# Kernel tuning notes

Measured on AMD Instinct MI355X. Metric: run time of the kernel, lower is better.

Reference implementation:

```python
import math
import jax, jax.numpy as jnp
import numpy as np

B, T, C, H = 2, 2048, 1024, 16
D = C // H


def _slopes(n):
    def p2(m):
        start = 2 ** (-(2 ** -(math.log2(m) - 3)))
        return [start * start ** i for i in range(m)]
    if math.log2(n).is_integer():
        return p2(n)
    c = 2 ** math.floor(math.log2(n))
    return p2(c) + _slopes(2 * c)[0::2][: n - c]


def setup_inputs() -> dict:
    key = jax.random.key(0)
    ks = jax.random.split(key, 9)
    std = 0.02
    x = jax.random.normal(ks[0], (B, T, C), dtype=jnp.float32)
    Wq = std * jax.random.normal(ks[1], (C, C), dtype=jnp.float32)
    Wk = std * jax.random.normal(ks[2], (C, C), dtype=jnp.float32)
    Wv = std * jax.random.normal(ks[3], (C, C), dtype=jnp.float32)
    # fc_resid init: std 0.02/sqrt(num_layers)
    Wo = (std / math.sqrt(24.0)) * jax.random.normal(ks[4], (C, C), dtype=jnp.float32)
    bq = jnp.zeros((C,), jnp.float32)
    bk = jnp.zeros((C,), jnp.float32)
    bv = jnp.zeros((C,), jnp.float32)
    bo = jnp.zeros((C,), jnp.float32)
    return {"x": x, "Wq": Wq, "bq": bq, "Wk": Wk, "bk": bk,
            "Wv": Wv, "bv": bv, "Wo": Wo, "bo": bo}


def reference(x, Wq, bq, Wk, bk, Wv, bv, Wo, bo):
    # projections -> [B, T, H, D]
    q = (x @ Wq + bq).reshape(B, T, H, D)
    k = (x @ Wk + bk).reshape(B, T, H, D)
    v = (x @ Wv + bv).reshape(B, T, H, D)

    scale = 1.0 / math.sqrt(D)
    att = jnp.einsum("bqhd,bkhd->bhqk", q, k) * scale  # [B,H,T,T]

    slopes = jnp.asarray(_slopes(H), dtype=jnp.float32)  # [H]
    i = jnp.arange(T)
    rel = i[None, :] - i[None, :].T  # rel[i,j] = j - i
    causal = rel <= 0  # j <= i
    # alibi bias: -tril(i - j) = tril(j - i), scaled per head
    alibi = slopes[:, None, None] * jnp.where(causal, rel, 0).astype(jnp.float32)

    att = att + alibi[None]  # broadcast over batch
    att = jnp.where(causal[None, None], att, -jnp.inf)
    att = jax.nn.softmax(att, axis=-1)

    y = jnp.einsum("bhqk,bkhd->bqhd", att, v).reshape(B, T, C)
    return y @ Wo + bo  # dropout p=0 (eval) is identity
```

## Files before the change

### kernel.cpp

```cpp
#include <hip/hip_runtime.h>
#include <hip/hip_bf16.h>

typedef __bf16 bf16;
typedef __bf16 bf16x4 __attribute__((ext_vector_type(4)));
typedef __bf16 bf16x8 __attribute__((ext_vector_type(8)));
typedef float floatx4 __attribute__((ext_vector_type(4)));
typedef short short4_ __attribute__((ext_vector_type(4)));

#define B_ 2
#define T_ 2048
#define C_ 1024
#define H_ 16
#define D_ 64
#define M_ 4096
#define QK_LD 2048

__device__ __forceinline__ void load_lds16(const void* g, void* l) {
  __builtin_amdgcn_global_load_lds(
      (const __attribute__((address_space(1))) unsigned int*)g,
      (__attribute__((address_space(3))) unsigned int*)l, 16, 0, 0);
}

__device__ __forceinline__ floatx4 mfma16(bf16x4 a, bf16x4 b, floatx4 c) {
#if __has_builtin(__builtin_amdgcn_mfma_f32_16x16x16_bf16)
  return __builtin_amdgcn_mfma_f32_16x16x16_bf16(a, b, c, 0, 0, 0);
#else
  return __builtin_amdgcn_mfma_f32_16x16x16bf16_1k(
      __builtin_bit_cast(short4_, a), __builtin_bit_cast(short4_, b), c, 0, 0, 0);
#endif
}

__device__ __forceinline__ bf16x4 lo4(bf16x8 v) {
  return __builtin_shufflevector(v, v, 0, 1, 2, 3);
}
__device__ __forceinline__ bf16x4 hi4(bf16x8 v) {
  return __builtin_shufflevector(v, v, 4, 5, 6, 7);
}

struct PrepArgs { const float* w[4]; bf16* wt[4]; const float* x; bf16* xb; };

__global__ __launch_bounds__(256)
void prep(PrepArgs p) {
  const int bid = blockIdx.x;
  if (bid < 4096) {
    __shared__ float tile[32][33];
    const int z = bid >> 10, xy = bid & 1023;
    const int bx = xy & 31, by = xy >> 5;
    const float* in = p.w[z];
    bf16* out = p.wt[z];
    int tx = threadIdx.x & 31, ty = threadIdx.x >> 5;
    int n0 = bx * 32, k0 = by * 32;
#pragma unroll
    for (int j = 0; j < 32; j += 8)
      tile[ty + j][tx] = in[(size_t)(k0 + ty + j) * C_ + n0 + tx];
    __syncthreads();
#pragma unroll
    for (int j = 0; j < 32; j += 8)
      out[(size_t)(n0 + ty + j) * C_ + k0 + tx] = (bf16)tile[tx][ty + j];
  } else {
    int i = ((bid - 4096) * 256 + threadIdx.x) * 8;
    float4 a = *(const float4*)(p.x + i);
    float4 b = *(const float4*)(p.x + i + 4);
    bf16x8 o;
    o[0] = (bf16)a.x; o[1] = (bf16)a.y; o[2] = (bf16)a.z; o[3] = (bf16)a.w;
    o[4] = (bf16)b.x; o[5] = (bf16)b.y; o[6] = (bf16)b.z; o[7] = (bf16)b.w;
    *(bf16x8*)(p.xb + i) = o;
  }
}

struct GQ {
  const bf16* A; const bf16* Bt;
  const float* bias[3];
  bf16* Cout; bf16* vt; int N; int K;
};

__global__ __launch_bounds__(256, 2)
void gemm128(GQ g) {
  __shared__ __align__(16) bf16 As[128 * 64];
  __shared__ __align__(16) bf16 Bs[128 * 64];
  const int tid = threadIdx.x;
  const int wave = tid >> 6, lane = tid & 63;
  const int quad = lane >> 4, l16 = lane & 15;
  const int id = blockIdx.x;
  const int xcd = id & 7, pos = id >> 3;
  const int mI = pos / 3, nl = pos - mI * 3;
  const int m0 = mI * 128, n0 = (xcd * 3 + nl) * 128;
  const int wm = (wave >> 1) * 64, wn = (wave & 1) * 64;

  floatx4 acc[4][4] = {};

  int rA[4], cA[4];
#pragma unroll
  for (int t = 0; t < 4; ++t) {
    int pch = (wave * 4 + t) * 64 + lane;
    rA[t] = pch >> 3;
    cA[t] = (pch & 7) ^ (rA[t] & 7);
  }

  for (int k0 = 0; k0 < g.K; k0 += 64) {
    __syncthreads();
#pragma unroll
    for (int t = 0; t < 4; ++t) {
      load_lds16(g.A + (size_t)(m0 + rA[t]) * g.K + k0 + cA[t] * 8,
                 As + (wave * 4 + t) * 512);
      load_lds16(g.Bt + (size_t)(n0 + rA[t]) * g.K + k0 + cA[t] * 8,
                 Bs + (wave * 4 + t) * 512);
    }
    __builtin_amdgcn_s_waitcnt(0x0f70);
    __syncthreads();
#pragma unroll
    for (int s = 0; s < 2; ++s) {
      bf16x8 af[4], bfr[4];
#pragma unroll
      for (int i = 0; i < 4; ++i) {
        int mr = wm + i * 16 + l16;
        af[i] = *(const bf16x8*)(As + ((mr * 8) + ((s * 4 + quad) ^ (mr & 7))) * 8);
        int nr = wn + i * 16 + l16;
        bfr[i] = *(const bf16x8*)(Bs + ((nr * 8) + ((s * 4 + quad) ^ (nr & 7))) * 8);
      }
#pragma unroll
      for (int i = 0; i < 4; ++i)
#pragma unroll
        for (int j = 0; j < 4; ++j)
          acc[i][j] = __builtin_amdgcn_mfma_f32_16x16x32_bf16(af[i], bfr[j],
                                                              acc[i][j], 0, 0, 0);
    }
  }

  const bool vsplit = (n0 >= 2048);
#pragma unroll
  for (int j = 0; j < 4; ++j) {
    int col = n0 + wn + j * 16 + l16;
    const float* bp = g.bias[col >> 10];
    float bv = bp[col & 1023];
    if (vsplit) {
      int cv = col - 2048;
      bf16* dstb = g.vt + ((size_t)((m0 >> 11) * 16 + (cv >> 6)) * 64 + (cv & 63)) * (size_t)T_
                   + (m0 & 2047) + wm + quad * 8;
#pragma unroll
      for (int ii = 0; ii < 2; ++ii) {
        bf16x8 pk;
#pragma unroll
        for (int r = 0; r < 8; ++r)
          pk[r] = (bf16)(acc[ii * 2 + (r >> 2)][j][r & 3] + bv);
        *(bf16x8*)(dstb + ii * 32) = pk;
      }
    } else {
#pragma unroll
      for (int i = 0; i < 4; ++i) {
#pragma unroll
        for (int r = 0; r < 4; ++r) {
          int row = m0 + wm + i * 16 + quad * 4 + r;
          g.Cout[(size_t)row * g.N + col] = (bf16)(acc[i][j][r] + bv);
        }
      }
    }
  }
}

__global__ __launch_bounds__(256, 2)
void gemm_out(const bf16* __restrict__ A, const bf16* __restrict__ Bt,
              const float* __restrict__ bias, float* __restrict__ C) {
  __shared__ __align__(16) bf16 As[64 * 64];
  __shared__ __align__(16) bf16 Bs[128 * 64];
  const int tid = threadIdx.x;
  const int wave = tid >> 6, lane = tid & 63;
  const int quad = lane >> 4, l16 = lane & 15;
  const int id = blockIdx.x;
  const int m0 = (id >> 3) * 64, n0 = (id & 7) * 128;
  const int wm = (wave >> 1) * 32, wn = (wave & 1) * 64;

  floatx4 acc[2][4] = {};

  int rA[2], cA[2], rB[4], cB[4];
#pragma unroll
  for (int t = 0; t < 2; ++t) {
    int p = t * 256 + tid;
    rA[t] = p >> 3; cA[t] = (p & 7) ^ (rA[t] & 7);
  }
#pragma unroll
  for (int t = 0; t < 4; ++t) {
    int p = t * 256 + tid;
    rB[t] = p >> 3; cB[t] = (p & 7) ^ (rB[t] & 7);
  }

  for (int k0 = 0; k0 < 1024; k0 += 64) {
    __syncthreads();
#pragma unroll
    for (int t = 0; t < 2; ++t)
      load_lds16(A + (size_t)(m0 + rA[t]) * 1024 + k0 + cA[t] * 8,
                 As + t * 2048 + wave * 512);
#pragma unroll
    for (int t = 0; t < 4; ++t)
      load_lds16(Bt + (size_t)(n0 + rB[t]) * 1024 + k0 + cB[t] * 8,
                 Bs + t * 2048 + wave * 512);
    __builtin_amdgcn_s_waitcnt(0x0f70);
    __syncthreads();
#pragma unroll
    for (int s = 0; s < 2; ++s) {
      bf16x8 af[2], bfr[4];
#pragma unroll
      for (int i = 0; i < 2; ++i) {
        int mr = wm + i * 16 + l16;
        af[i] = *(const bf16x8*)(As + ((mr * 8) + ((s * 4 + quad) ^ (mr & 7))) * 8);
      }
#pragma unroll
      for (int j = 0; j < 4; ++j) {
        int nr = wn + j * 16 + l16;
        bfr[j] = *(const bf16x8*)(Bs + ((nr * 8) + ((s * 4 + quad) ^ (nr & 7))) * 8);
      }
#pragma unroll
      for (int i = 0; i < 2; ++i)
#pragma unroll
        for (int j = 0; j < 4; ++j)
          acc[i][j] = __builtin_amdgcn_mfma_f32_16x16x32_bf16(af[i], bfr[j],
                                                              acc[i][j], 0, 0, 0);
    }
  }

#pragma unroll
  for (int j = 0; j < 4; ++j) {
    int col = n0 + wn + j * 16 + l16;
    float bv = bias[col];
#pragma unroll
    for (int i = 0; i < 2; ++i)
#pragma unroll
      for (int r = 0; r < 4; ++r) {
        int row = m0 + wm + i * 16 + quad * 4 + r;
        C[(size_t)row * 1024 + col] = acc[i][j][r] + bv;
      }
  }
}

__global__ __launch_bounds__(512, 2)
void attn8(const bf16* __restrict__ qk, const bf16* __restrict__ vt,
           bf16* __restrict__ y, bf16* __restrict__ po, float* __restrict__ pl) {
  __shared__ __align__(16) bf16 smem[32768];
  const int tid = threadIdx.x, wave = tid >> 6, lane = tid & 63;
  const int quad = lane >> 4, l16 = lane & 15;
  const int qs = wave >> 1, kh = wave & 1;
  const int id = blockIdx.x;
  const int bh = (id & 7) * 4 + ((id >> 3) & 3);
  const int rem = id >> 5;
  const int p = rem >> 1;
  const bool roleB = rem & 1;
  const int b = bh >> 4, h = bh & 15;

  const float L2E = 1.4426950408889634f;
  const float slope2 = exp2f(-0.5f * (float)(h + 1)) * L2E;
  const float scl2 = 0.125f * L2E;
  const float M0 = 14.0f;

  bf16x4 onesA;
#pragma unroll
  for (int j = 0; j < 4; ++j) onesA[j] = (bf16)1.0f;

  const int rS = tid >> 3;
  const int cS = (tid & 7) ^ (rS & 7);
  const bf16* kbase = qk + (size_t)b * T_ * QK_LD + 1024 + h * 64;
  const bf16* vbase = vt + (size_t)bh * 64 * T_;

  float kc[2][4];
#pragma unroll
  for (int kt = 0; kt < 2; ++kt)
#pragma unroll
    for (int r = 0; r < 4; ++r)
      kc[kt][r] = slope2 * (float)(kt * 16 + quad * 4 + r);

  int qb_ = roleB ? (15 - p) : p;
  int t0_ = 0;
  int t1_ = roleB ? 17 : (2 * p + 2);
  int sg_ = roleB ? 0 : -1;

  for (int ph = 0;; ++ph) {
    const int w0 = qb_ * 128 + qs * 32;
    const int qi0 = w0 + l16;
    float qoff[2];
    qoff[0] = slope2 * (float)qi0 + M0;
    qoff[1] = qoff[0] + slope2 * 16.0f;

    bf16x8 qf[2][2];
#pragma unroll
    for (int qt = 0; qt < 2; ++qt)
#pragma unroll
      for (int s = 0; s < 2; ++s)
        qf[qt][s] = *(const bf16x8*)(qk +
            (size_t)(b * T_ + w0 + qt * 16 + l16) * QK_LD + h * 64 + s * 32 + quad * 8);

    floatx4 o[2][4];
#pragma unroll
    for (int qt = 0; qt < 2; ++qt)
#pragma unroll
      for (int n = 0; n < 4; ++n) o[qt][n] = (floatx4)0.f;
    floatx4 lacc[2];
    lacc[0] = (floatx4)0.f; lacc[1] = (floatx4)0.f;

    auto tilebody = [&](const bf16* Klc, const bf16* Vlc, int t) {
      const int kj0 = t * 64;
      bf16x8 kf[2][2];
#pragma unroll
      for (int ss = 0; ss < 2; ++ss)
#pragma unroll
        for (int kt = 0; kt < 2; ++kt) {
          const int krow = kh * 32 + kt * 16 + l16;
          kf[ss][kt] = *(const bf16x8*)(Klc + krow * 64 +
                                        (((ss * 4 + quad) ^ (krow & 7)) * 8));
        }
      bf16x8 vf8[4];
#pragma unroll
      for (int nt = 0; nt < 4; ++nt) {
        const int drow = nt * 16 + l16;
        vf8[nt] = *(const bf16x8*)(Vlc + drow * 64 +
                                   (((kh * 4 + quad) ^ (drow & 7)) * 8));
      }

      const int kbi = kj0 + kh * 32;
      const float kb = slope2 * (float)kbi;

      __builtin_amdgcn_s_setprio(1);
#pragma unroll
      for (int qt = 0; qt < 2; ++qt) {
        const int rb = w0 + qt * 16;
        floatx4 st[2] = {};
#pragma unroll
        for (int ss = 0; ss < 2; ++ss)
#pragma unroll
          for (int kt = 0; kt < 2; ++kt)
            st[kt] = __builtin_amdgcn_mfma_f32_16x16x32_bf16(kf[ss][kt], qf[qt][ss],
                                                             st[kt], 0, 0, 0);

        const float bb = kb - qoff[qt];
        const int qi = qi0 + qt * 16;
        bf16x4 pb[2];
        if (kbi + 31 > rb) {
#pragma unroll
          for (int kt = 0; kt < 2; ++kt) {
#pragma unroll
            for (int r = 0; r < 4; ++r) {
              float pv = __builtin_amdgcn_exp2f(
                  fmaf(st[kt][r], scl2, bb + kc[kt][r]));
              if (kbi + kt * 16 + quad * 4 + r > qi) pv = 0.f;
              pb[kt][r] = (bf16)pv;
            }
          }
        } else {
#pragma unroll
          for (int kt = 0; kt < 2; ++kt) {
#pragma unroll
            for (int r = 0; r < 4; ++r)
              pb[kt][r] = (bf16)__builtin_amdgcn_exp2f(
                  fmaf(st[kt][r], scl2, bb + kc[kt][r]));
          }
        }

        lacc[qt] = mfma16(onesA, pb[0], lacc[qt]);
        lacc[qt] = mfma16(onesA, pb[1], lacc[qt]);

#pragma unroll
        for (int nt = 0; nt < 4; ++nt) {
          o[qt][nt] = mfma16(lo4(vf8[nt]), pb[0], o[qt][nt]);
          o[qt][nt] = mfma16(hi4(vf8[nt]), pb[1], o[qt][nt]);
        }
      }
      __builtin_amdgcn_s_setprio(0);
    };

#pragma unroll
    for (int s2 = 0; s2 < 2; ++s2) {
      load_lds16(kbase + (size_t)((t0_ + s2) * 64 + rS) * QK_LD + cS * 8,
                 smem + s2 * 4096 + wave * 512);
      load_lds16(vbase + (size_t)rS * T_ + (t0_ + s2) * 64 + cS * 8,
                 smem + 16384 + s2 * 4096 + wave * 512);
    }
    __builtin_amdgcn_s_waitcnt(0x0f70);
    __syncthreads();

    const int len = t1_ - t0_;
    const int npair = len >> 1;
    const int nit = (len + 1) >> 1;
    for (int it = 0; it < npair; ++it) {
      const int cur = it & 1;
      if (it + 1 < nit) {
        const int nt0 = t0_ + 2 * it + 2;
#pragma unroll
        for (int s2 = 0; s2 < 2; ++s2) {
          load_lds16(kbase + (size_t)((nt0 + s2) * 64 + rS) * QK_LD + cS * 8,
                     smem + (cur ^ 1) * 8192 + s2 * 4096 + wave * 512);
          load_lds16(vbase + (size_t)rS * T_ + (nt0 + s2) * 64 + cS * 8,
                     smem + 16384 + (cur ^ 1) * 8192 + s2 * 4096 + wave * 512);
        }
      }
      tilebody(smem + cur * 8192,        smem + 16384 + cur * 8192,        t0_ + 2 * it);
      tilebody(smem + cur * 8192 + 4096, smem + 16384 + cur * 8192 + 4096, t0_ + 2 * it + 1);
      __builtin_amdgcn_s_waitcnt(0x0f70);
      __syncthreads();
    }
    if (len & 1) {
      const int cur = npair & 1;
      tilebody(smem + cur * 8192, smem + 16384 + cur * 8192, t1_ - 1);
      __syncthreads();
    }

    float* Cb = (float*)smem;
    float lsum[2];
#pragma unroll
    for (int qt = 0; qt < 2; ++qt) lsum[qt] = lacc[qt][0];
    if (kh == 1) {
#pragma unroll
      for (int qt = 0; qt < 2; ++qt) {
#pragma unroll
        for (int n = 0; n < 4; ++n)
          *(floatx4*)(Cb + (((qs * 2 + qt) * 4 + n) * 64 + lane) * 4) = o[qt][n];
        Cb[8192 + (qs * 2 + qt) * 64 + lane] = lsum[qt];
      }
    }
    __syncthreads();
    if (kh == 0) {
#pragma unroll
      for (int qt = 0; qt < 2; ++qt) {
#pragma unroll
        for (int n = 0; n < 4; ++n)
          o[qt][n] += *(const floatx4*)(Cb + (((qs * 2 + qt) * 4 + n) * 64 + lane) * 4);
        lsum[qt] += Cb[8192 + (qs * 2 + qt) * 64 + lane];
      }

      if (sg_ < 0) {
#pragma unroll
        for (int qt = 0; qt < 2; ++qt) {
          const float inv = 1.f / lsum[qt];
          bf16* yp = y + (size_t)(b * T_ + w0 + qt * 16 + l16) * C_ + h * 64 + quad * 4;
#pragma unroll
          for (int nt = 0; nt < 4; ++nt) {
            bf16x4 pk;
#pragma unroll
            for (int r = 0; r < 4; ++r) pk[r] = (bf16)(o[qt][nt][r] * inv);
            *(bf16x4*)(yp + nt * 16) = pk;
          }
        }
      } else {
        const int pid = (bh * 8 + (qb_ - 8)) * 2 + sg_;
        bf16* pob = po + (size_t)pid * 8192;
#pragma unroll
        for (int qt = 0; qt < 2; ++qt) {
#pragma unroll
          for (int half = 0; half < 2; ++half) {
            bf16x8 pk;
#pragma unroll
            for (int jj = 0; jj < 8; ++jj)
              pk[jj] = (bf16)o[qt][half * 2 + (jj >> 2)][jj & 3];
            *(bf16x8*)(pob + (qt * 2 + half) * 2048 + (qs * 64 + lane) * 8) = pk;
          }
          if (quad == 0)
            pl[pid * 128 + qs * 32 + qt * 16 + l16] = lsum[qt];
        }
      }
    }
    __syncthreads();

    if (roleB || ph == 1) break;
    qb_ = 15 - p; t0_ = 17; t1_ = 32 - 2 * p; sg_ = 1;
  }
}

__global__ __launch_bounds__(256)
void combine(const bf16* __restrict__ po, const float* __restrict__ pl,
             bf16* __restrict__ y) {
  const int x = blockIdx.x;
  const int bh = x >> 3, qb = (x & 7) + 8;
  const int b = bh >> 4, h = bh & 15;
  const int pid0 = (bh * 8 + (qb - 8)) * 2;
  const bf16* p0 = po + (size_t)pid0 * 8192;
  const bf16* p1 = p0 + 8192;
  const int t = threadIdx.x;
  const int qs = t >> 6, quad = (t >> 4) & 3, l16 = t & 15;

  float linv[2];
  int row[2];
#pragma unroll
  for (int qt = 0; qt < 2; ++qt) {
    row[qt] = qs * 32 + qt * 16 + l16;
    linv[qt] = 1.f / (pl[pid0 * 128 + row[qt]] + pl[(pid0 + 1) * 128 + row[qt]]);
  }

#pragma unroll
  for (int qt = 0; qt < 2; ++qt)
#pragma unroll
    for (int half = 0; half < 2; ++half) {
      bf16x8 a = *(const bf16x8*)(p0 + (qt * 2 + half) * 2048 + t * 8);
      bf16x8 c = *(const bf16x8*)(p1 + (qt * 2 + half) * 2048 + t * 8);
#pragma unroll
      for (int g = 0; g < 2; ++g) {
        bf16x4 outv;
#pragma unroll
        for (int r = 0; r < 4; ++r)
          outv[r] = (bf16)(((float)a[g * 4 + r] + (float)c[g * 4 + r]) * linv[qt]);
        const int col = (half * 2 + g) * 16 + quad * 4;
        *(bf16x4*)(y + (size_t)(b * T_ + qb * 128 + row[qt]) * C_ + h * 64 + col) = outv;
      }
    }
}

extern "C" void kernel_launch(void* const* d_in, const int* in_sizes, int n_in,
                              void* d_out, int out_size, void* d_ws, size_t ws_size,
                              hipStream_t stream) {
  const float* x  = (const float*)d_in[0];
  const float* Wq = (const float*)d_in[1];
  const float* bq = (const float*)d_in[2];
  const float* Wk = (const float*)d_in[3];
  const float* bk = (const float*)d_in[4];
  const float* Wv = (const float*)d_in[5];
  const float* bv = (const float*)d_in[6];
  const float* Wo = (const float*)d_in[7];
  const float* bo = (const float*)d_in[8];

  bf16* ws  = (bf16*)d_ws;
  bf16* WtQ = ws;
  bf16* WtK = WtQ + (size_t)C_ * C_;
  bf16* WtV = WtK + (size_t)C_ * C_;
  bf16* WtO = WtV + (size_t)C_ * C_;
  bf16* xb  = WtO + (size_t)C_ * C_;
  bf16* qkb = xb + (size_t)M_ * C_;
  bf16* vtb = qkb + (size_t)M_ * 2 * C_;
  bf16* yb  = vtb + (size_t)M_ * C_;
  bf16* pob = yb + (size_t)M_ * C_;
  float* plb = (float*)(pob + (size_t)512 * 8192);

  PrepArgs pp;
  pp.w[0] = Wq; pp.w[1] = Wk; pp.w[2] = Wv; pp.w[3] = Wo;
  pp.wt[0] = WtQ; pp.wt[1] = WtK; pp.wt[2] = WtV; pp.wt[3] = WtO;
  pp.x = x; pp.xb = xb;
  prep<<<dim3(4096 + M_ * C_ / (256 * 8)), 256, 0, stream>>>(pp);

  GQ gq;
  gq.A = xb; gq.Bt = WtQ;
  gq.bias[0] = bq; gq.bias[1] = bk; gq.bias[2] = bv;
  gq.Cout = qkb; gq.vt = vtb; gq.N = 2 * C_; gq.K = C_;
  gemm128<<<dim3(768), 256, 0, stream>>>(gq);

  attn8<<<dim3(512), 512, 0, stream>>>(qkb, vtb, yb, pob, plb);
  combine<<<dim3(32 * 8), 256, 0, stream>>>(pob, plb, yb);

  gemm_out<<<dim3(512), 256, 0, stream>>>(yb, WtO, bo, (float*)d_out);
}
```

Baseline: 180.1 us.

## Shrink attention LDS to single-tile double buffer to fit three blocks per CU

The attention kernel previously staged two 64-key K/V tiles per double-buffer stage, using 64KB of LDS. It now stages one tile per stage, cutting LDS to about 34KB, and raises the launch-bounds min-blocks hint from 2 to 3 so more blocks can be resident per CU. The cost is twice as many barriers and waitcnts per key range and less prefetch lookahead per iteration. The higher occupancy hint may also push register pressure into spills.

```diff
diff --git a/kernel.cpp b/kernel.cpp
--- a/kernel.cpp
+++ b/kernel.cpp
@@ -232,10 +232,10 @@
   }
 }
 
-__global__ __launch_bounds__(512, 2)
+__global__ __launch_bounds__(512, 3)
 void attn8(const bf16* __restrict__ qk, const bf16* __restrict__ vt,
            bf16* __restrict__ y, bf16* __restrict__ po, float* __restrict__ pl) {
-  __shared__ __align__(16) bf16 smem[32768];
+  __shared__ __align__(16) bf16 smem[17408];
   const int tid = threadIdx.x, wave = tid >> 6, lane = tid & 63;
   const int quad = lane >> 4, l16 = lane & 15;
   const int qs = wave >> 1, kh = wave & 1;
@@ -365,39 +365,25 @@
       __builtin_amdgcn_s_setprio(0);
     };
 
-#pragma unroll
-    for (int s2 = 0; s2 < 2; ++s2) {
-      load_lds16(kbase + (size_t)((t0_ + s2) * 64 + rS) * QK_LD + cS * 8,
-                 smem + s2 * 4096 + wave * 512);
-      load_lds16(vbase + (size_t)rS * T_ + (t0_ + s2) * 64 + cS * 8,
-                 smem + 16384 + s2 * 4096 + wave * 512);
-    }
+    load_lds16(kbase + (size_t)(t0_ * 64 + rS) * QK_LD + cS * 8,
+               smem + wave * 512);
+    load_lds16(vbase + (size_t)rS * T_ + t0_ * 64 + cS * 8,
+               smem + 8192 + wave * 512);
     __builtin_amdgcn_s_waitcnt(0x0f70);
     __syncthreads();
 
     const int len = t1_ - t0_;
-    const int npair = len >> 1;
-    const int nit = (len + 1) >> 1;
-    for (int it = 0; it < npair; ++it) {
+    for (int it = 0; it < len; ++it) {
       const int cur = it & 1;
-      if (it + 1 < nit) {
-        const int nt0 = t0_ + 2 * it + 2;
-#pragma unroll
-        for (int s2 = 0; s2 < 2; ++s2) {
-          load_lds16(kbase + (size_t)((nt0 + s2) * 64 + rS) * QK_LD + cS * 8,
-                     smem + (cur ^ 1) * 8192 + s2 * 4096 + wave * 512);
-          load_lds16(vbase + (size_t)rS * T_ + (nt0 + s2) * 64 + cS * 8,
-                     smem + 16384 + (cur ^ 1) * 8192 + s2 * 4096 + wave * 512);
-        }
-      }
-      tilebody(smem + cur * 8192,        smem + 16384 + cur * 8192,        t0_ + 2 * it);
-      tilebody(smem + cur * 8192 + 4096, smem + 16384 + cur * 8192 + 4096, t0_ + 2 * it + 1);
+      if (it + 1 < len) {
+        const int nt = t0_ + it + 1;
+        load_lds16(kbase + (size_t)(nt * 64 + rS) * QK_LD + cS * 8,
+                   smem + (cur ^ 1) * 4096 + wave * 512);
+        load_lds16(vbase + (size_t)rS * T_ + nt * 64 + cS * 8,
+                   smem + 8192 + (cur ^ 1) * 4096 + wave * 512);
+      }
+      tilebody(smem + cur * 4096, smem + 8192 + cur * 4096, t0_ + it);
       __builtin_amdgcn_s_waitcnt(0x0f70);
-      __syncthreads();
-    }
-    if (len & 1) {
-      const int cur = npair & 1;
-      tilebody(smem + cur * 8192, smem + 16384 + cur * 8192, t1_ - 1);
       __syncthreads();
     }
 
```

Result: slower. 186.4 us (+3.5%).
